# Performance work log

Measured on AMD Instinct MI355X. Metric: run time of the kernel, lower is better.

Reference implementation:

```python
import jax, jax.numpy as jnp
import numpy as np
from jax import lax

EPS = 1e-5
K_UP = 5
RATIO = 2
PAD = 2


def conv1x1(x, w):
    # x: (B,C,H,W), w: (O,C)
    return jnp.einsum('bchw,oc->bohw', x, w)


def bn(x, g, b, m, v):
    inv = g / jnp.sqrt(v + EPS)
    return x * inv[None, :, None, None] + (b - m * inv)[None, :, None, None]


def relu6(x):
    return jnp.clip(x, 0.0, 6.0)


def carafe_down(x, wc, bc, we, be):
    # content-aware reassembly kernels
    y = conv1x1(x, wc) + bc[None, :, None, None]              # (B, 64, H, W)
    y = lax.conv_general_dilated(
        y, we, window_strides=(RATIO, RATIO), padding=[(PAD, PAD), (PAD, PAD)],
        dimension_numbers=('NCHW', 'OIHW', 'NCHW')) + be[None, :, None, None]
    w = jax.nn.softmax(y, axis=1)                              # (B, 25, Ho, Wo)
    B, C, H, W = x.shape
    Ho, Wo = H // RATIO, W // RATIO
    xp = jnp.pad(x, ((0, 0), (0, 0), (PAD, PAD), (PAD, PAD)))
    out = jnp.zeros((B, C, Ho, Wo), x.dtype)
    k = 0
    for i in range(K_UP):
        for j in range(K_UP):
            patch = xp[:, :, i:i + RATIO * Ho:RATIO, j:j + RATIO * Wo:RATIO]
            out = out + patch * w[:, k][:, None]
            k += 1
    return out


def setup_inputs() -> dict:
    key = jax.random.key(0)
    ks = jax.random.split(key, 20)
    B, INP, H, W = 8, 64, 112, 112
    OUP, HID, CMID = 128, 384, 64

    def bn_params(k, c):
        k1, k2, k3, k4 = jax.random.split(k, 4)
        return (jax.random.uniform(k1, (c,), jnp.float32, 0.5, 1.5),
                jax.random.normal(k2, (c,), jnp.float32) * 0.1,
                jax.random.normal(k3, (c,), jnp.float32) * 0.1,
                jax.random.uniform(k4, (c,), jnp.float32, 0.5, 1.5))
    g1, b1, m1, v1 = bn_params(ks[1], HID)
    g2, b2, m2, v2 = bn_params(ks[2], HID)
    g3, b3, m3, v3 = bn_params(ks[3], OUP)
    return {
        'x': jax.random.normal(ks[0], (B, INP, H, W), jnp.float32),
        'w1': jax.random.normal(ks[4], (HID, INP), jnp.float32) / np.sqrt(INP),
        'g1': g1, 'b1': b1, 'm1': m1, 'v1': v1,
        'wc': jax.random.normal(ks[5], (CMID, HID), jnp.float32) / np.sqrt(HID),
        'bc': jax.random.normal(ks[6], (CMID,), jnp.float32) * 0.01,
        'we': jax.random.normal(ks[7], (K_UP**2, CMID, 5, 5), jnp.float32) / np.sqrt(CMID * 25),
        'be': jax.random.normal(ks[8], (K_UP**2,), jnp.float32) * 0.01,
        'g2': g2, 'b2': b2, 'm2': m2, 'v2': v2,
        'w2': jax.random.normal(ks[9], (OUP, HID), jnp.float32) / np.sqrt(HID),
        'g3': g3, 'b3': b3, 'm3': m3, 'v3': v3,
    }


def reference(x, w1, g1, b1, m1, v1, wc, bc, we, be, g2, b2, m2, v2, w2, g3, b3, m3, v3):
    # stride-2 InvertedResidualBlockCarafe (no identity): 1x1 expand -> BN -> ReLU6
    # -> CARAFE_downsample -> BN -> ReLU6 -> 1x1 project -> BN
    h = relu6(bn(conv1x1(x, w1), g1, b1, m1, v1))
    h = relu6(bn(carafe_down(h, wc, bc, we, be), g2, b2, m2, v2))
    return bn(conv1x1(h, w2), g3, b3, m3, v3)
```

## Files before the change

### kernel.cpp

```cpp
#include <hip/hip_runtime.h>
#include <hip/hip_bf16.h>
#include <type_traits>

#define EPS 1e-5f

typedef _Float16 half8 __attribute__((ext_vector_type(8)));
typedef _Float16 half4 __attribute__((ext_vector_type(4)));
typedef _Float16 half2v __attribute__((ext_vector_type(2)));
typedef float f32x4 __attribute__((ext_vector_type(4)));

__global__ __launch_bounds__(256) void fold_k(
    const float* __restrict__ w1, const float* __restrict__ g1, const float* __restrict__ b1,
    const float* __restrict__ m1, const float* __restrict__ v1,
    const float* __restrict__ wc,
    const float* __restrict__ g2, const float* __restrict__ b2,
    const float* __restrict__ m2, const float* __restrict__ v2,
    const float* __restrict__ w2, const float* __restrict__ g3, const float* __restrict__ b3,
    const float* __restrict__ m3, const float* __restrict__ v3,
    _Float16* __restrict__ w1h, float* __restrict__ bias1,
    _Float16* __restrict__ wch,
    _Float16* __restrict__ w2h, float* __restrict__ bias3,
    float* __restrict__ s2, float* __restrict__ t2) {
  int i = blockIdx.x * 256 + threadIdx.x;
  if (i < 384 * 64) {
    int o = i >> 6;
    float inv = g1[o] / sqrtf(v1[o] + EPS);
    w1h[i] = (_Float16)(w1[i] * inv);
  }
  if (i < 64 * 384) wch[i] = (_Float16)wc[i];
  if (i < 128 * 384) {
    int o = i / 384;
    float inv = g3[o] / sqrtf(v3[o] + EPS);
    w2h[i] = (_Float16)(w2[i] * inv);
  }
  if (i < 384) {
    float inv = g1[i] / sqrtf(v1[i] + EPS);
    bias1[i] = b1[i] - m1[i] * inv;
    float inv2 = g2[i] / sqrtf(v2[i] + EPS);
    s2[i] = inv2;
    t2[i] = b2[i] - m2[i] * inv2;
  }
  if (i < 128) {
    float inv = g3[i] / sqrtf(v3[i] + EPS);
    bias3[i] = b3[i] - m3[i] * inv;
  }
}

__global__ __launch_bounds__(256) void wtrans2_k(const float* __restrict__ we,
                                                 _Float16* __restrict__ wa) {
  int i = blockIdx.x * 256 + threadIdx.x;
  if (i >= 51200) return;
  int j = i & 7;
  int lane = (i >> 3) & 63;
  int f = i >> 9;
  int ocf = f & 1;
  int tap = (f >> 1) % 25;
  int ph = f / 50;
  int oc = ocf * 16 + (lane & 15);
  int cm = ph * 32 + (lane >> 4) * 8 + j;
  float v = (oc < 25) ? we[((size_t)oc * 64 + cm) * 25 + tap] : 0.f;
  wa[i] = (_Float16)v;
}

__global__ __launch_bounds__(256) void fused1_k(
    const float* __restrict__ x, const _Float16* __restrict__ w1h,
    const float* __restrict__ bias1, const _Float16* __restrict__ wch,
    const float* __restrict__ bc, _Float16* __restrict__ hq,
    _Float16* __restrict__ yq) {
  __shared__ __align__(16) unsigned char smem_raw[63488];
  _Float16 (*xh)[40]  = (_Float16 (*)[40])smem_raw;
  _Float16 (*hT)[76]  = (_Float16 (*)[76])(smem_raw + 5120);
  _Float16 (*oTy)[72] = (_Float16 (*)[72])(smem_raw + 5120);

  const int tid = threadIdx.x;
  const int lane = tid & 63;
  const int w = tid >> 6;
  const int l15 = lane & 15;
  const int g = lane >> 4;
  const int wpx = w * 16;
  const int p0 = blockIdx.x * 64;
  const int b = blockIdx.y;
  const float* inb = x + (size_t)b * 64 * 12544 + p0;

  f32x4 acc1[24];
#pragma unroll
  for (int fo = 0; fo < 24; ++fo) acc1[fo] = (f32x4){0.f, 0.f, 0.f, 0.f};

  for (int kk = 0; kk < 64; kk += 32) {
    __syncthreads();
#pragma unroll
    for (int i = 0; i < 2; ++i) {
      int slot = tid + 256 * i;
      int px = slot & 63;
      int kq = slot >> 6;
      const float* src = inb + (size_t)(kk + kq * 4) * 12544 + px;
      half4 v = {(_Float16)src[0], (_Float16)src[12544],
                 (_Float16)src[2 * 12544], (_Float16)src[3 * 12544]};
      *(half4*)&xh[px][kq * 4] = v;
    }
    __syncthreads();
    half8 xb = *(const half8*)&xh[wpx + l15][g * 8];
#pragma unroll
    for (int fo = 0; fo < 24; ++fo) {
      half8 a = *(const half8*)&w1h[(size_t)(fo * 16 + l15) * 64 + kk + g * 8];
      acc1[fo] = __builtin_amdgcn_mfma_f32_16x16x32_f16(a, xb, acc1[fo], 0, 0, 0);
    }
  }

#pragma unroll
  for (int fo = 0; fo < 24; ++fo) {
#pragma unroll
    for (int r = 0; r < 4; ++r) {
      int oc = fo * 16 + g * 4 + r;
      float v = acc1[fo][r] + bias1[oc];
      v = fminf(fmaxf(v, 0.f), 6.f);
      hT[oc][wpx + l15] = (_Float16)v;
    }
  }
  __syncthreads();

#pragma unroll
  for (int i = 0; i < 12; ++i) {
    int idx = tid + 256 * i;
    int row = idx >> 3, j8 = idx & 7;
    half8 v = *(const half8*)&hT[row][j8 * 8];
    *(half8*)&hq[(size_t)(b * 384 + row) * 12544 + p0 + j8 * 8] = v;
  }

  f32x4 acc2[4];
#pragma unroll
  for (int fo2 = 0; fo2 < 4; ++fo2) acc2[fo2] = (f32x4){0.f, 0.f, 0.f, 0.f};
#pragma unroll
  for (int ks = 0; ks < 12; ++ks) {
    half8 bf;
#pragma unroll
    for (int j = 0; j < 8; ++j) bf[j] = hT[ks * 32 + g * 8 + j][wpx + l15];
#pragma unroll
    for (int fo2 = 0; fo2 < 4; ++fo2) {
      half8 a = *(const half8*)&wch[(size_t)(fo2 * 16 + l15) * 384 + ks * 32 + g * 8];
      acc2[fo2] = __builtin_amdgcn_mfma_f32_16x16x32_f16(a, bf, acc2[fo2], 0, 0, 0);
    }
  }
  __syncthreads();

#pragma unroll
  for (int fo2 = 0; fo2 < 4; ++fo2) {
#pragma unroll
    for (int r = 0; r < 4; ++r) {
      int oc2 = fo2 * 16 + g * 4 + r;
      oTy[oc2][wpx + l15] = (_Float16)(acc2[fo2][r] + bc[oc2]);
    }
  }
  __syncthreads();
#pragma unroll
  for (int i = 0; i < 2; ++i) {
    int slot = tid + 256 * i;
    int row = slot >> 3, j8 = slot & 7;
    half8 v = *(const half8*)&oTy[row][j8 * 8];
    *(half8*)&yq[(size_t)(b * 64 + row) * 12544 + p0 + j8 * 8] = v;
  }
}

template <int IC, int NPF, int ACT, typename TI, typename TO>
__global__ __launch_bounds__(256) void gemm16_k(
    const TI* __restrict__ in, const _Float16* __restrict__ wh,
    const float* __restrict__ bias, TO* __restrict__ out, int npx) {
  constexpr int BPX = NPF * 64;
  constexpr int L2B = (BPX == 128) ? 7 : 6;
  constexpr int PAD = 16 / sizeof(TO);
  constexpr int CH = 16 / sizeof(TO);
  constexpr int SPAN = NPF * 16;
  constexpr int LPO = SPAN / CH;
  constexpr int OCPI = 64 / LPO;
  using vec16 = std::conditional_t<std::is_same_v<TO, _Float16>, half8, float4>;

  __shared__ _Float16 xh[BPX][40];
  __shared__ TO oT[64][BPX + PAD];

  const int tid = threadIdx.x;
  const int lane = tid & 63;
  const int w = tid >> 6;
  const int l15 = lane & 15;
  const int g = lane >> 4;
  const int wpx = w * SPAN;
  const int p0 = blockIdx.x * BPX;
  const int oc0 = blockIdx.y * 64;
  const int b = blockIdx.z;
  const int OCT = gridDim.y * 64;
  const TI* inb = in + (size_t)b * IC * npx + p0;

  f32x4 acc[4][NPF];
#pragma unroll
  for (int fo = 0; fo < 4; ++fo)
#pragma unroll
    for (int pf = 0; pf < NPF; ++pf)
      acc[fo][pf] = (f32x4){0.f, 0.f, 0.f, 0.f};

  for (int kk = 0; kk < IC; kk += 32) {
    __syncthreads();
    half8 a[4];
#pragma unroll
    for (int fo = 0; fo < 4; ++fo)
      a[fo] = *(const half8*)&wh[(size_t)(oc0 + fo * 16 + l15) * IC + kk + g * 8];
#pragma unroll
    for (int i = 0; i < NPF * 2; ++i) {
      int slot = tid + 256 * i;
      int px = slot & (BPX - 1);
      int kq = slot >> L2B;
      const TI* src = inb + (size_t)(kk + kq * 4) * npx + px;
      half4 v = {(_Float16)src[0], (_Float16)src[npx],
                 (_Float16)src[2 * npx], (_Float16)src[3 * npx]};
      *(half4*)&xh[px][kq * 4] = v;
    }
    __syncthreads();
    half8 xb[NPF];
#pragma unroll
    for (int pf = 0; pf < NPF; ++pf)
      xb[pf] = *(const half8*)&xh[wpx + pf * 16 + l15][g * 8];
#pragma unroll
    for (int fo = 0; fo < 4; ++fo)
#pragma unroll
      for (int pf = 0; pf < NPF; ++pf)
        acc[fo][pf] = __builtin_amdgcn_mfma_f32_16x16x32_f16(
            a[fo], xb[pf], acc[fo][pf], 0, 0, 0);
  }

#pragma unroll
  for (int fo = 0; fo < 4; ++fo) {
#pragma unroll
    for (int r = 0; r < 4; ++r) {
      float bz = bias[oc0 + fo * 16 + g * 4 + r];
#pragma unroll
      for (int pf = 0; pf < NPF; ++pf) {
        float v = acc[fo][pf][r] + bz;
        if (ACT) v = fminf(fmaxf(v, 0.f), 6.f);
        oT[fo * 16 + g * 4 + r][wpx + pf * 16 + l15] = (TO)v;
      }
    }
  }
#pragma unroll
  for (int i = 0; i < LPO; ++i) {
    int oc = i * OCPI + lane / LPO;
    int pxo = (lane % LPO) * CH;
    vec16 v = *(const vec16*)&oT[oc][wpx + pxo];
    *(vec16*)&out[((size_t)b * OCT + oc0 + oc) * npx + p0 + wpx + pxo] = v;
  }
}

__global__ __launch_bounds__(256) void mask_conv5_k(
    const _Float16* __restrict__ y, const _Float16* __restrict__ wa,
    float* __restrict__ lg) {
  __shared__ _Float16 ysh[32][5][136];
  const int ho = blockIdx.x;
  const int b = blockIdx.y;
  const int tid = threadIdx.x;
  const int lane = tid & 63;
  const int w = tid >> 6;
  const int l15 = lane & 15;
  const int g = lane >> 4;
  const int wo = w * 16 + l15;
  const int woe = (wo < 56) ? wo : 55;
  const int ci0 = 2 * woe + 6;

  for (int i = tid; i < 640; i += 256) {
    int ch = i / 20; int rem = i - ch * 20; int ri = rem / 4; int q = rem & 3;
    *(uint*)&ysh[ch][ri][q * 2] = 0u;
  }
  for (int i = tid; i < 1280; i += 256) {
    int ch = i / 40; int rem = i - ch * 40; int ri = rem / 8; int q = rem & 7;
    *(uint*)&ysh[ch][ri][120 + q * 2] = 0u;
  }

  f32x4 acc[2] = {(f32x4){0.f, 0.f, 0.f, 0.f}, (f32x4){0.f, 0.f, 0.f, 0.f}};

  for (int ph = 0; ph < 2; ++ph) {
    __syncthreads();
    for (int i = tid; i < 2240; i += 256) {
      int ch = i / 70;
      int rem = i - ch * 70;
      int ri = rem / 14;
      int j8 = rem - ri * 14;
      int hi = 2 * ho - 2 + ri;
      half8 v = {0, 0, 0, 0, 0, 0, 0, 0};
      if ((unsigned)hi < 112u)
        v = *(const half8*)&y[((size_t)(b * 64 + ph * 32 + ch) * 112 + hi) * 112 + j8 * 8];
      *(half8*)&ysh[ch][ri][8 + j8 * 8] = v;
    }
    __syncthreads();

    const _Float16* wap = wa + (size_t)ph * 25600;
#pragma unroll
    for (int di = 0; di < 5; ++di) {
      half2v pa[8], pb[8];
      _Float16 pc[8];
#pragma unroll
      for (int j = 0; j < 8; ++j) {
        pa[j] = *(const half2v*)&ysh[g * 8 + j][di][ci0];
        pb[j] = *(const half2v*)&ysh[g * 8 + j][di][ci0 + 2];
        pc[j] = ysh[g * 8 + j][di][ci0 + 4];
      }
#pragma unroll
      for (int dj = 0; dj < 5; ++dj) {
        half8 bf;
#pragma unroll
        for (int j = 0; j < 8; ++j)
          bf[j] = (dj == 0) ? pa[j][0]
                : (dj == 1) ? pa[j][1]
                : (dj == 2) ? pb[j][0]
                : (dj == 3) ? pb[j][1]
                            : pc[j];
        const int tap = di * 5 + dj;
        half8 a0 = *(const half8*)&wap[(tap * 2 + 0) * 512 + lane * 8];
        half8 a1 = *(const half8*)&wap[(tap * 2 + 1) * 512 + lane * 8];
        acc[0] = __builtin_amdgcn_mfma_f32_16x16x32_f16(a0, bf, acc[0], 0, 0, 0);
        acc[1] = __builtin_amdgcn_mfma_f32_16x16x32_f16(a1, bf, acc[1], 0, 0, 0);
      }
    }
  }

  if (wo < 56) {
#pragma unroll
    for (int ocf = 0; ocf < 2; ++ocf)
#pragma unroll
      for (int r = 0; r < 4; ++r) {
        int oc = ocf * 16 + g * 4 + r;
        if (oc < 25)
          lg[((size_t)b * 25 + oc) * 3136 + ho * 56 + wo] = acc[ocf][r];
      }
  }
}

__global__ __launch_bounds__(256) void softmax3_k(
    const float* __restrict__ lg, const float* __restrict__ be,
    float* __restrict__ msk) {
  int idx = blockIdx.x * 256 + threadIdx.x;
  if (idx >= 8 * 3136) return;
  int b = idx / 3136, sp = idx - (idx / 3136) * 3136;
  float v[25];
  float mx = -1e30f;
#pragma unroll
  for (int k = 0; k < 25; ++k) {
    float s = lg[((size_t)b * 25 + k) * 3136 + sp] + be[k];
    v[k] = s;
    mx = fmaxf(mx, s);
  }
  float s = 0.f;
#pragma unroll
  for (int k = 0; k < 25; ++k) {
    v[k] = __expf(v[k] - mx);
    s += v[k];
  }
  float inv = 1.0f / s;
#pragma unroll
  for (int k = 0; k < 25; ++k)
    msk[((size_t)b * 25 + k) * 3136 + sp] = v[k] * inv;
}

__device__ __forceinline__ void stage_pair(float dst[2][19][120],
                                           const _Float16* __restrict__ hbase,
                                           int ho0, int tid) {
  for (int i = tid; i < 2 * 19 * 14; i += 512) {
    int ch = i / 266;
    int rem = i - ch * 266;
    int rr = rem / 14;
    int j8 = rem - rr * 14;
    int hi = 2 * ho0 - 2 + rr;
    float4 lo = {0.f, 0.f, 0.f, 0.f}, hi4 = {0.f, 0.f, 0.f, 0.f};
    if ((unsigned)hi < 112u) {
      half8 v = *(const half8*)&hbase[(size_t)ch * 12544 + hi * 112 + j8 * 8];
      lo = (float4){(float)v[0], (float)v[1], (float)v[2], (float)v[3]};
      hi4 = (float4){(float)v[4], (float)v[5], (float)v[6], (float)v[7]};
    }
    *(float4*)&dst[ch][rr][4 + j8 * 8] = lo;
    *(float4*)&dst[ch][rr][8 + j8 * 8] = hi4;
  }
}

__global__ __launch_bounds__(512) void carafe3_k(
    const _Float16* __restrict__ h, const float* __restrict__ msk,
    const float* __restrict__ s2, const float* __restrict__ t2,
    _Float16* __restrict__ h2) {
  __shared__ float ys[2][2][19][120];
  const int hx = blockIdx.x;
  const int b  = blockIdx.y;
  const int cz = blockIdx.z;
  const int ho0 = hx * 8;
  const int tid = threadIdx.x;
  const int r = tid / 56;
  const int c = tid - r * 56;
  const int c0 = cz * 24;

  for (int i = tid; i < 2 * 2 * 19 * 8; i += 512) {
    int bufi = i / 304;
    int rem = i - bufi * 304;
    int ch = rem / 152;
    int rem2 = rem - ch * 152;
    int rr = rem2 / 8;
    int p = rem2 - rr * 8;
    int col = (p < 4) ? p : (112 + p);
    ys[bufi][ch][rr][col] = 0.f;
  }

  float m[25];
  if (tid < 448) {
    const float* mp = msk + (size_t)b * 25 * 3136 + (ho0 + r) * 56 + c;
#pragma unroll
    for (int k = 0; k < 25; ++k) m[k] = mp[(size_t)k * 3136];
  }
  __syncthreads();

  stage_pair(ys[0], h + (size_t)(b * 384 + c0) * 12544, ho0, tid);
  __syncthreads();

#pragma unroll
  for (int p = 0; p < 12; ++p) {
    const int bf = p & 1;
    if (p + 1 < 12)
      stage_pair(ys[bf ^ 1], h + (size_t)(b * 384 + c0 + 2 * (p + 1)) * 12544,
                 ho0, tid);
    if (tid < 448) {
#pragma unroll
      for (int cl = 0; cl < 2; ++cl) {
        const int cc = c0 + 2 * p + cl;
        float acc = 0.f;
#pragma unroll
        for (int di = 0; di < 5; ++di) {
          const float* row = &ys[bf][cl][2 * r + di][2 * c + 2];
          float2 a01 = *(const float2*)&row[0];
          float2 a23 = *(const float2*)&row[2];
          float a4 = row[4];
          acc = fmaf(a01.x, m[di * 5 + 0], acc);
          acc = fmaf(a01.y, m[di * 5 + 1], acc);
          acc = fmaf(a23.x, m[di * 5 + 2], acc);
          acc = fmaf(a23.y, m[di * 5 + 3], acc);
          acc = fmaf(a4,    m[di * 5 + 4], acc);
        }
        float o = s2[cc] * acc + t2[cc];
        h2[((size_t)(b * 384 + cc) * 56 + ho0 + r) * 56 + c] =
            (_Float16)fminf(fmaxf(o, 0.f), 6.f);
      }
    }
    __syncthreads();
  }
}

extern "C" void kernel_launch(void* const* d_in, const int* in_sizes, int n_in,
                              void* d_out, int out_size, void* d_ws, size_t ws_size,
                              hipStream_t stream) {
  const float* x  = (const float*)d_in[0];
  const float* w1 = (const float*)d_in[1];
  const float* g1 = (const float*)d_in[2];
  const float* b1 = (const float*)d_in[3];
  const float* m1 = (const float*)d_in[4];
  const float* v1 = (const float*)d_in[5];
  const float* wc = (const float*)d_in[6];
  const float* bc = (const float*)d_in[7];
  const float* we = (const float*)d_in[8];
  const float* be = (const float*)d_in[9];
  const float* g2 = (const float*)d_in[10];
  const float* b2 = (const float*)d_in[11];
  const float* m2 = (const float*)d_in[12];
  const float* v2 = (const float*)d_in[13];
  const float* w2 = (const float*)d_in[14];
  const float* g3 = (const float*)d_in[15];
  const float* b3 = (const float*)d_in[16];
  const float* m3 = (const float*)d_in[17];
  const float* v3 = (const float*)d_in[18];
  float* out = (float*)d_out;

  _Float16* hq  = (_Float16*)d_ws;
  _Float16* yq  = hq + 38535168;
  _Float16* h2q = yq + 6422528;
  float* lg     = (float*)(h2q + 9633792);
  float* mskf   = lg + 627200;
  float* bias1  = mskf + 627200;
  float* bias3  = bias1 + 384;
  float* s2     = bias3 + 128;
  float* t2     = s2 + 384;
  _Float16* w1h = (_Float16*)(t2 + 384);
  _Float16* wch = w1h + 24576;
  _Float16* w2h = wch + 24576;
  _Float16* wa  = w2h + 49152;

  fold_k<<<192, 256, 0, stream>>>(w1, g1, b1, m1, v1, wc, g2, b2, m2, v2,
                                  w2, g3, b3, m3, v3,
                                  w1h, bias1, wch, w2h, bias3, s2, t2);
  wtrans2_k<<<200, 256, 0, stream>>>(we, wa);

  fused1_k<<<dim3(196, 8), 256, 0, stream>>>(x, w1h, bias1, wch, bc, hq, yq);

  mask_conv5_k<<<dim3(56, 8), 256, 0, stream>>>(yq, wa, lg);
  softmax3_k<<<98, 256, 0, stream>>>(lg, be, mskf);

  carafe3_k<<<dim3(7, 8, 16), 512, 0, stream>>>(hq, mskf, s2, t2, h2q);

  gemm16_k<384, 1, 0, _Float16, float>
      <<<dim3(49, 2, 8), 256, 0, stream>>>(h2q, w2h, bias3, out, 3136);
}
```

Measured before the change: 181.6 us.

## Stream expanded activations through a double-buffered LDS chunk to cut shared memory

The fused expand/reduce kernel used to stage the full 384-channel activation tile in LDS, about 62 KB per block. It now applies bias and ReLU6 and stores 32 channels at a time into a small ping-pong buffer. Each chunk is written to global memory and fed into the second MFMA GEMM before the next chunk is produced. This brings LDS use down to about 15 KB per block so more blocks can be resident per CU, at the cost of twelve extra block-wide barriers inside the loop.

```diff
diff --git a/kernel.cpp b/kernel.cpp
--- a/kernel.cpp
+++ b/kernel.cpp
@@ -67,10 +67,8 @@
     const float* __restrict__ bias1, const _Float16* __restrict__ wch,
     const float* __restrict__ bc, _Float16* __restrict__ hq,
     _Float16* __restrict__ yq) {
-  __shared__ __align__(16) unsigned char smem_raw[63488];
-  _Float16 (*xh)[40]  = (_Float16 (*)[40])smem_raw;
-  _Float16 (*hT)[76]  = (_Float16 (*)[76])(smem_raw + 5120);
-  _Float16 (*oTy)[72] = (_Float16 (*)[72])(smem_raw + 5120);
+  __shared__ _Float16 xh[64][40];
+  __shared__ _Float16 cbuf[64][76];
 
   const int tid = threadIdx.x;
   const int lane = tid & 63;
@@ -106,38 +104,38 @@
       acc1[fo] = __builtin_amdgcn_mfma_f32_16x16x32_f16(a, xb, acc1[fo], 0, 0, 0);
     }
   }
-
-#pragma unroll
-  for (int fo = 0; fo < 24; ++fo) {
-#pragma unroll
-    for (int r = 0; r < 4; ++r) {
-      int oc = fo * 16 + g * 4 + r;
-      float v = acc1[fo][r] + bias1[oc];
-      v = fminf(fmaxf(v, 0.f), 6.f);
-      hT[oc][wpx + l15] = (_Float16)v;
-    }
-  }
   __syncthreads();
 
-#pragma unroll
-  for (int i = 0; i < 12; ++i) {
-    int idx = tid + 256 * i;
-    int row = idx >> 3, j8 = idx & 7;
-    half8 v = *(const half8*)&hT[row][j8 * 8];
-    *(half8*)&hq[(size_t)(b * 384 + row) * 12544 + p0 + j8 * 8] = v;
-  }
-
   f32x4 acc2[4];
 #pragma unroll
   for (int fo2 = 0; fo2 < 4; ++fo2) acc2[fo2] = (f32x4){0.f, 0.f, 0.f, 0.f};
-#pragma unroll
-  for (int ks = 0; ks < 12; ++ks) {
+
+  const int srow = tid >> 3, sj8 = tid & 7;
+
+#pragma unroll
+  for (int ck = 0; ck < 12; ++ck) {
+    _Float16 (*cb)[76] = (_Float16 (*)[76])cbuf[(ck & 1) * 32];
+#pragma unroll
+    for (int q = 0; q < 2; ++q) {
+#pragma unroll
+      for (int r = 0; r < 4; ++r) {
+        int ocl = q * 16 + g * 4 + r;
+        float v = acc1[ck * 2 + q][r] + bias1[ck * 32 + ocl];
+        v = fminf(fmaxf(v, 0.f), 6.f);
+        cb[ocl][wpx + l15] = (_Float16)v;
+      }
+    }
+    __syncthreads();
+    {
+      half8 v = *(const half8*)&cb[srow][sj8 * 8];
+      *(half8*)&hq[(size_t)(b * 384 + ck * 32 + srow) * 12544 + p0 + sj8 * 8] = v;
+    }
     half8 bf;
 #pragma unroll
-    for (int j = 0; j < 8; ++j) bf[j] = hT[ks * 32 + g * 8 + j][wpx + l15];
+    for (int j = 0; j < 8; ++j) bf[j] = cb[g * 8 + j][wpx + l15];
 #pragma unroll
     for (int fo2 = 0; fo2 < 4; ++fo2) {
-      half8 a = *(const half8*)&wch[(size_t)(fo2 * 16 + l15) * 384 + ks * 32 + g * 8];
+      half8 a = *(const half8*)&wch[(size_t)(fo2 * 16 + l15) * 384 + ck * 32 + g * 8];
       acc2[fo2] = __builtin_amdgcn_mfma_f32_16x16x32_f16(a, bf, acc2[fo2], 0, 0, 0);
     }
   }
@@ -148,7 +146,7 @@
 #pragma unroll
     for (int r = 0; r < 4; ++r) {
       int oc2 = fo2 * 16 + g * 4 + r;
-      oTy[oc2][wpx + l15] = (_Float16)(acc2[fo2][r] + bc[oc2]);
+      cbuf[oc2][wpx + l15] = (_Float16)(acc2[fo2][r] + bc[oc2]);
     }
   }
   __syncthreads();
@@ -156,7 +154,7 @@
   for (int i = 0; i < 2; ++i) {
     int slot = tid + 256 * i;
     int row = slot >> 3, j8 = slot & 7;
-    half8 v = *(const half8*)&oTy[row][j8 * 8];
+    half8 v = *(const half8*)&cbuf[row][j8 * 8];
     *(half8*)&yq[(size_t)(b * 64 + row) * 12544 + p0 + j8 * 8] = v;
   }
 }
```

Result: no change. 183.4 us (+1.0%).
